# Performance work log

Hardware: AMD Instinct MI355X
Metric: run time of the kernel (lower is better)

The kernel has to match this reference:

```python
import jax, jax.numpy as jnp
import numpy as np

WIN = 12     # SAMv3 window_size
HEADS = 8    # num_heads

def _window(t, win=WIN):
    B, H, W, C = t.shape
    t = t.reshape(B, H // win, win, W // win, win, C).transpose(0, 1, 3, 2, 4, 5)
    return t.reshape(B, (H // win) * (W // win), win * win, C)

def _unwindow(t, H, W, win=WIN):
    B, nW, S, C = t.shape
    t = t.reshape(B, H // win, W // win, win, win, C).transpose(0, 1, 3, 2, 4, 5)
    return t.reshape(B, H, W, C)

def _sam(fq, fkv, bias, wq, wk, wv, wo, bo):
    # Windowed, masked cross-frame multi-head attention (SAMv3).
    # fq, fkv: (B, C, H, W); bias: (B, nW, 1, 1, S) additive mask bias.
    B, C, H, W = fq.shape
    hd = C // HEADS
    scale = hd ** -0.5
    q = _window(jnp.einsum('bchw,cd->bhwd', fq, wq))   # (B,nW,S,C)
    k = _window(jnp.einsum('bchw,cd->bhwd', fkv, wk))
    v = _window(jnp.einsum('bchw,cd->bhwd', fkv, wv))
    nW, S = q.shape[1], q.shape[2]
    q = q.reshape(B, nW, S, HEADS, hd)
    k = k.reshape(B, nW, S, HEADS, hd)
    v = v.reshape(B, nW, S, HEADS, hd)
    attn = jnp.einsum('bnqhd,bnkhd->bnhqk', q, k) * scale + bias
    attn = jax.nn.softmax(attn, axis=-1)
    out = jnp.einsum('bnhqk,bnkhd->bnqhd', attn, v).reshape(B, nW, S, C)
    out = out @ wo + bo
    return _unwindow(out, H, W).transpose(0, 3, 1, 2)  # (B, C, H, W)

def setup_inputs() -> dict:
    key = jax.random.key(0)
    B, C, T, H, W = 2, 384, 2, 192, 192
    ks = jax.random.split(key, 16)
    d = {}
    d['x'] = jax.random.normal(ks[0], (B, C, T, H, W), jnp.float32)
    d['mask'] = jax.random.randint(ks[1], (B, T, 1, H, W), 0, 2, jnp.int32)
    names = ['sam1_wq', 'sam1_wk', 'sam1_wv', 'sam1_wo',
             'sam2_wq', 'sam2_wk', 'sam2_wv', 'sam2_wo',
             'proj1_w', 'proj2_w']
    for i, n in enumerate(names):
        d[n] = jax.random.normal(ks[2 + i], (C, C), jnp.float32) * 0.02
    d['sam1_bo'] = jnp.zeros((C,), jnp.float32)
    d['sam2_bo'] = jnp.zeros((C,), jnp.float32)
    d['proj1_b'] = jnp.zeros((C,), jnp.float32)
    d['proj2_b'] = jnp.zeros((C,), jnp.float32)
    return d

def reference(x, mask, sam1_wq, sam1_wk, sam1_wv, sam1_wo, sam1_bo,
              sam2_wq, sam2_wk, sam2_wv, sam2_wo, sam2_bo,
              proj1_w, proj1_b, proj2_w, proj2_b):
    # x: (B, C, T=2, H, W); mask: (B, T, 1, H, W)
    f1 = x[:, :, 0]
    f2 = x[:, :, 1]
    m = mask[:, 1, 0][..., None]                      # (B, H, W, 1), frame-2 mask
    mw = _window(m)[..., 0]                           # (B, nW, S)
    bias = jnp.where(mw == 0, -1e9, 0.0).astype(x.dtype)[:, :, None, None, :]
    o1 = _sam(f1, f2, bias, sam1_wq, sam1_wk, sam1_wv, sam1_wo, sam1_bo)
    x1 = jnp.einsum('bchw,dc->bdhw', o1, proj1_w) + proj1_b[None, :, None, None]
    o2 = _sam(f2, f1, bias, sam2_wq, sam2_wk, sam2_wv, sam2_wo, sam2_bo)
    x2 = jnp.einsum('bchw,dc->bdhw', o2, proj2_w) + proj2_b[None, :, None, None]
    return jnp.concatenate([x1[:, :, None], x2[:, :, None]], axis=2)  # (B, C, 2, H, W)
```

## Files before the change

kernel.cpp:

```cpp
#include <hip/hip_runtime.h>
#include <stdint.h>

typedef __attribute__((ext_vector_type(8))) short bf16x8;
typedef __attribute__((ext_vector_type(4))) float f32x4;

#define HW    36864
#define CCH   384
#define NPIX  73728
#define W2    147456

__device__ __forceinline__ unsigned short f2bf(float f) {
  unsigned u = __builtin_bit_cast(unsigned, f);
  u += 0x7FFFu + ((u >> 16) & 1u);
  return (unsigned short)(u >> 16);
}

typedef const unsigned int __attribute__((address_space(1)))* gas1_t;
typedef unsigned int __attribute__((address_space(3)))* las3_t;
__device__ __forceinline__ void gload16(const void* g, void* l) {
  __builtin_amdgcn_global_load_lds((gas1_t)g, (las3_t)l, 16, 0, 0);
}


__global__ void k_wt(const float* __restrict__ w0, const float* __restrict__ w1,
                     const float* __restrict__ w2, const float* __restrict__ w3,
                     const float* __restrict__ w4, const float* __restrict__ w5,
                     unsigned short* __restrict__ wt) {
  int idx = blockIdx.x * 256 + threadIdx.x;
  int w = blockIdx.y;
  const float* W;
  switch (w) { case 0: W = w0; break; case 1: W = w1; break;
               case 2: W = w2; break; case 3: W = w3; break;
               case 4: W = w4; break; default: W = w5; break; }
  const int slotmap[6] = {0, 4, 5, 3, 1, 2};
  int slot = slotmap[w];
  int c = idx / 384, d = idx % 384;
  wt[(size_t)slot * W2 + (size_t)d * 384 + c] = f2bf(W[(size_t)c * 384 + d]);
}

__global__ void k_wf(const float* __restrict__ wo1, const float* __restrict__ pj1,
                     const float* __restrict__ wo2, const float* __restrict__ pj2,
                     unsigned short* __restrict__ wfT) {
  int idx = blockIdx.x * 256 + threadIdx.x;
  int s = blockIdx.y;
  const float* wo = s ? wo2 : wo1;
  const float* pj = s ? pj2 : pj1;
  int d = idx / 384, e = idx % 384;
  float acc = 0.f;
  for (int c = 0; c < 384; ++c) acc += pj[d * 384 + c] * wo[e * 384 + c];
  wfT[(size_t)s * W2 + (size_t)d * 384 + e] = f2bf(acc);
}

__global__ void k_bf(const float* __restrict__ bo1, const float* __restrict__ pj1,
                     const float* __restrict__ pb1, const float* __restrict__ bo2,
                     const float* __restrict__ pj2, const float* __restrict__ pb2,
                     float* __restrict__ bfused) {
  int t = threadIdx.x;
  int s = t / 384, d = t % 384;
  const float* bo = s ? bo2 : bo1;
  const float* pj = s ? pj2 : pj1;
  const float* pb = s ? pb2 : pb1;
  float acc = pb[d];
  for (int c = 0; c < 384; ++c) acc += pj[d * 384 + c] * bo[c];
  bfused[t] = acc;
}

__global__ __launch_bounds__(256) void k_tx(const float* __restrict__ x,
                                            unsigned short* __restrict__ xbf) {
  __shared__ float tile[64][65];
  int p0 = blockIdx.x * 64;
  int c0 = blockIdx.y * 64;
  int bt = blockIdx.z;
  int b = bt >> 1, t = bt & 1;
  int tid = threadIdx.x;
  int cl = tid >> 2;
  int pq = (tid & 3) * 4;
  const float* src = x + (((size_t)b * CCH + (c0 + cl)) * 2 + t) * HW + p0;
#pragma unroll
  for (int i = 0; i < 4; ++i) {
    int p_l = pq + i * 16;
    float4 v = *reinterpret_cast<const float4*>(src + p_l);
    tile[cl][p_l + 0] = v.x; tile[cl][p_l + 1] = v.y;
    tile[cl][p_l + 2] = v.z; tile[cl][p_l + 3] = v.w;
  }
  __syncthreads();
  int pl = tid >> 2;
  int cq = (tid & 3) * 16;
  unsigned short* dst = xbf + ((size_t)(t * 2 + b) * HW + p0 + pl) * CCH + c0 + cq;
  bf16x8 o0, o1;
#pragma unroll
  for (int j = 0; j < 8; ++j) o0[j] = (short)f2bf(tile[cq + j][pl]);
#pragma unroll
  for (int j = 0; j < 8; ++j) o1[j] = (short)f2bf(tile[cq + 8 + j][pl]);
  *reinterpret_cast<bf16x8*>(dst) = o0;
  *reinterpret_cast<bf16x8*>(dst + 8) = o1;
}

__global__ __launch_bounds__(512) void gemm_qkv(
    const unsigned short* __restrict__ xbf,
    const unsigned short* __restrict__ wt,
    unsigned short* __restrict__ qb0,
    unsigned short* __restrict__ qb1,
    unsigned short* __restrict__ kvb0,
    unsigned short* __restrict__ kvb1,
    float oscale) {
  __shared__ __align__(16) unsigned short Lsh[3][24576];
  const int tid = threadIdx.x;
  const int lane = tid & 63;
  const int wid = tid >> 6;
  const int wr = wid >> 1, wc = wid & 1;
  const int r15 = lane & 15, g = lane >> 4;

  const int gx = gridDim.x;
  const int nwg = gx * gridDim.y;
  const int bid = blockIdx.x + blockIdx.y * gx;
  const int chunk = nwg >> 3;
  const int l = (bid & 7) * chunk + (bid >> 3);
  const int bx = l % gx, by = l / gx;

  const int f = (by >= 288) ? 1 : 0;
  const int m0 = (by - f * 288) * 256;
  const int n0 = bx * 128;

  const unsigned short* A  = xbf + (size_t)f * NPIX * 384;
  const unsigned short* Bt = wt + (size_t)f * 3 * W2;
  unsigned short* Cq  = f ? qb1 : qb0;
  unsigned short* Ckv = f ? kvb0 : kvb1;

  const int gsl = (tid & 7) ^ ((tid >> 3) & 7);
  const unsigned short* srcA = A + (size_t)(m0 + (tid >> 3)) * 384 + gsl * 8;
  const unsigned short* srcB = Bt + (size_t)(n0 + (tid >> 3)) * 384 + gsl * 8;
  const int wu = tid & ~63;

  f32x4 acc[4][4];
  f32x4 zero4 = {0.f, 0.f, 0.f, 0.f};
#pragma unroll
  for (int a = 0; a < 4; ++a)
#pragma unroll
    for (int b = 0; b < 4; ++b) acc[a][b] = zero4;

#define STAGE_H0(buf, kt) do {                                         \
    size_t ko = (size_t)(kt) * 64;                                     \
    gload16(srcA + ko,            &Lsh[(buf)][(wu) * 8]);              \
    gload16(srcA + 64*384 + ko,   &Lsh[(buf)][(512 + wu) * 8]);        \
    gload16(srcB + ko,            &Lsh[(buf)][16384 + (wu) * 8]);      \
  } while (0)
#define STAGE_H1(buf, kt) do {                                         \
    size_t ko = (size_t)(kt) * 64;                                     \
    gload16(srcA + 128*384 + ko,  &Lsh[(buf)][(1024 + wu) * 8]);       \
    gload16(srcA + 192*384 + ko,  &Lsh[(buf)][(1536 + wu) * 8]);       \
    gload16(srcB + 64*384 + ko,   &Lsh[(buf)][16384 + (512 + wu) * 8]);\
  } while (0)

  const int rsw = r15 & 7;

#define PHASE(buf, ks, DO_STAGE, nbuf, kt2, END) do {                           \
    bf16x8 af[4], bfv[4];                                                       \
    _Pragma("unroll")                                                           \
    for (int a = 0; a < 4; ++a) {                                               \
      int row = wr * 64 + a * 16 + r15;                                         \
      af[a] = *(const bf16x8*)&Lsh[(buf)][row * 64 + (((ks)*4 + g) ^ rsw) * 8]; \
    }                                                                           \
    _Pragma("unroll")                                                           \
    for (int b = 0; b < 4; ++b) {                                               \
      int row = wc * 64 + b * 16 + r15;                                         \
      bfv[b] = *(const bf16x8*)&Lsh[(buf)][16384 + row * 64 + (((ks)*4 + g) ^ rsw) * 8];\
    }                                                                           \
    if (DO_STAGE == 1) STAGE_H0(nbuf, kt2);                                     \
    if (DO_STAGE == 2) STAGE_H1(nbuf, kt2);                                     \
    __builtin_amdgcn_s_barrier();                                               \
    asm volatile("s_waitcnt lgkmcnt(0)" ::: "memory");                          \
    __builtin_amdgcn_s_setprio(1);                                              \
    _Pragma("unroll")                                                           \
    for (int a = 0; a < 4; ++a)                                                 \
      _Pragma("unroll")                                                         \
      for (int b = 0; b < 4; ++b)                                               \
        acc[a][b] = __builtin_amdgcn_mfma_f32_16x16x32_bf16(af[a], bfv[b], acc[a][b], 0, 0, 0);\
    __builtin_amdgcn_s_setprio(0);                                              \
    if (END == 1) { asm volatile("s_waitcnt vmcnt(6)" ::: "memory"); }          \
    if (END != 2) { __builtin_amdgcn_s_barrier(); }                             \
  } while (0)

  STAGE_H0(0, 0); STAGE_H1(0, 0);
  STAGE_H0(1, 1); STAGE_H1(1, 1);
  asm volatile("s_waitcnt vmcnt(6)" ::: "memory");
  __builtin_amdgcn_s_barrier();

#pragma unroll
  for (int t = 0; t < 4; ++t) {
    const int buf = t % 3, nbuf = (t + 2) % 3;
    PHASE(buf, 0, 1, nbuf, t + 2, 0);
    PHASE(buf, 1, 2, nbuf, t + 2, 1);
  }
  PHASE(1, 0, 0, 0, 0, 0);
  PHASE(1, 1, 0, 0, 0, 2);
  __syncthreads();
  PHASE(2, 0, 0, 0, 0, 2);
  asm volatile("s_waitcnt lgkmcnt(0)" ::: "memory");
  PHASE(2, 1, 0, 0, 0, 2);
#undef STAGE_H0
#undef STAGE_H1
#undef PHASE

  unsigned short* Cp;
  int ldc2, ncol0;
  float sc;
  if (n0 < 384) { Cp = Cq;  ldc2 = 384; ncol0 = n0;       sc = oscale; }
  else          { Cp = Ckv; ldc2 = 768; ncol0 = n0 - 384; sc = 1.0f;   }
#pragma unroll
  for (int a = 0; a < 4; ++a) {
    size_t rbase = (size_t)(m0 + wr * 64 + a * 16 + g * 4) * ldc2;
#pragma unroll
    for (int b = 0; b < 4; ++b) {
      int n = ncol0 + wc * 64 + b * 16 + r15;
      unsigned short* cp = Cp + rbase + n;
#pragma unroll
      for (int r = 0; r < 4; ++r) cp[(size_t)r * ldc2] = f2bf(acc[a][b][r] * sc);
    }
  }
}

__global__ __launch_bounds__(256) void gemm_out(
    const unsigned short* __restrict__ wfT,
    const unsigned short* __restrict__ ob0,
    const unsigned short* __restrict__ ob1,
    float* __restrict__ Cf,
    const float* __restrict__ bfu) {
  __shared__ __align__(16) unsigned short Lsh[3][8192];
  const int tid = threadIdx.x;
  const int lane = tid & 63;
  const int wid = tid >> 6, wr = wid >> 1, wc = wid & 1;

  const int gx = gridDim.x, gy = gridDim.y;
  const int nwg = gx * gy * gridDim.z;
  const int bid = blockIdx.x + (blockIdx.y + blockIdx.z * gy) * gx;
  const int chunk = nwg >> 3;
  const int l = (bid & 7) * chunk + (bid >> 3);
  const int bx = l % gx;
  const int by = (l / gx) % gy;
  const int s  = l / (gx * gy);

  const unsigned short* A  = wfT + (size_t)s * W2;
  const unsigned short* Bt = s ? ob1 : ob0;
  const float* bias = bfu + s * 384;

  const int m0 = bx * 128;
  const int n0 = by * 128;
  const int r15 = lane & 15, g = lane >> 4;

  const int u1 = tid + 256;
  const unsigned short* srcA0 = A + (size_t)(m0 + (tid >> 2)) * 384 + (((tid & 3) ^ ((tid >> 3) & 3)) << 3);
  const unsigned short* srcA1 = A + (size_t)(m0 + (u1 >> 2)) * 384 + (((u1 & 3) ^ ((u1 >> 3) & 3)) << 3);
  const unsigned short* srcB0 = Bt + (size_t)(n0 + (tid >> 2)) * 384 + (((tid & 3) ^ ((tid >> 3) & 3)) << 3);
  const unsigned short* srcB1 = Bt + (size_t)(n0 + (u1 >> 2)) * 384 + (((u1 & 3) ^ ((u1 >> 3) & 3)) << 3);
  const int wbase = (tid & ~63) * 8;

  f32x4 acc[4][4];
  f32x4 zero4 = {0.f, 0.f, 0.f, 0.f};
#pragma unroll
  for (int a = 0; a < 4; ++a)
#pragma unroll
    for (int b = 0; b < 4; ++b) acc[a][b] = zero4;

  const int swzr = (g ^ ((r15 >> 1) & 3)) << 3;

#define STAGE(buf, kt) do {                                  \
    int ke = (kt) * 32;                                      \
    gload16(srcA0 + ke, &Lsh[(buf)][wbase]);                 \
    gload16(srcA1 + ke, &Lsh[(buf)][2048 + wbase]);          \
    gload16(srcB0 + ke, &Lsh[(buf)][4096 + wbase]);          \
    gload16(srcB1 + ke, &Lsh[(buf)][6144 + wbase]);          \
  } while (0)

#define COMPUTE(buf) do {                                                       \
    bf16x8 af[4], bfv[4];                                                       \
    _Pragma("unroll")                                                           \
    for (int a = 0; a < 4; ++a)                                                 \
      af[a] = *(const bf16x8*)&Lsh[(buf)][(wr * 64 + a * 16 + r15) * 32 + swzr];\
    _Pragma("unroll")                                                           \
    for (int b = 0; b < 4; ++b)                                                 \
      bfv[b] = *(const bf16x8*)&Lsh[(buf)][4096 + (wc * 64 + b * 16 + r15) * 32 + swzr];\
    _Pragma("unroll")                                                           \
    for (int a = 0; a < 4; ++a)                                                 \
      _Pragma("unroll")                                                         \
      for (int b = 0; b < 4; ++b)                                               \
        acc[a][b] = __builtin_amdgcn_mfma_f32_16x16x32_bf16(af[a], bfv[b], acc[a][b], 0, 0, 0);\
  } while (0)

  STAGE(0, 0);
  STAGE(1, 1);
#pragma unroll
  for (int kt = 0; kt < 11; ++kt) {
    asm volatile("s_waitcnt vmcnt(4)" ::: "memory");
    __builtin_amdgcn_s_barrier();
    asm volatile("" ::: "memory");
    if (kt < 10) STAGE((kt + 2) % 3, kt + 2);
    COMPUTE(kt % 3);
  }
  __syncthreads();
  COMPUTE(11 % 3);
#undef STAGE
#undef COMPUTE

  int bb = n0 / HW;
#pragma unroll
  for (int a = 0; a < 4; ++a) {
    int d = m0 + wr * 64 + a * 16 + g * 4;
#pragma unroll
    for (int b = 0; b < 4; ++b) {
      int n = n0 + wc * 64 + b * 16 + r15;
      int p = n - bb * HW;
#pragma unroll
      for (int r = 0; r < 4; ++r) {
        float v = acc[a][b][r] + bias[d + r];
        Cf[(((size_t)bb * CCH + (d + r)) * 2 + s) * HW + p] = v;
      }
    }
  }
}

__global__ __launch_bounds__(512, 2) void attn_kernel(
    const unsigned short* __restrict__ qb0,
    const unsigned short* __restrict__ qb1,
    const unsigned short* __restrict__ kvb0,
    const unsigned short* __restrict__ kvb1,
    const int* __restrict__ mask,
    unsigned short* __restrict__ ob0,
    unsigned short* __restrict__ ob1) {
  __shared__ __align__(16) unsigned short P[8][16][168];
  __shared__ int ptab[144];
  const int n = blockIdx.x, b = blockIdx.y, s = blockIdx.z;
  const unsigned short* q  = s ? qb1 : qb0;
  const unsigned short* kv = s ? kvb1 : kvb0;
  unsigned short* obuf = s ? ob1 : ob0;
  const int tid = threadIdx.x;
  const int h = tid >> 6, lane = tid & 63;
  const int c15 = lane & 15, g = lane >> 4;
  const int wy = n >> 4, wx = n & 15;
  const size_t rowbase = (size_t)b * HW;
  const int* mrow = mask + (size_t)(b * 2 + 1) * HW;

  if (tid < 144)
    ptab[tid] = (wy * 12 + tid / 12) * 192 + wx * 12 + tid % 12;

  for (int idx = lane; idx < 16 * 24; idx += 64)
    P[h][idx / 24][144 + (idx % 24)] = 0;
  __syncthreads();

  float biasv[9];
#pragma unroll
  for (int nt = 0; nt < 9; ++nt)
    biasv[nt] = (mrow[ptab[nt * 16 + c15]] == 0) ? -1e9f : 0.0f;

  bf16x8 zfrag = {0, 0, 0, 0, 0, 0, 0, 0};
  f32x4 zero4 = {0.f, 0.f, 0.f, 0.f};

  bf16x8 kf0[9], kf1[9];
#pragma unroll
  for (int nt = 0; nt < 9; ++nt) {
    const unsigned short* kp = kv + (rowbase + ptab[nt * 16 + c15]) * 768 + h * 48;
    kf0[nt] = *(const bf16x8*)(kp + g * 8);
    kf1[nt] = zfrag;
    if (g < 2) kf1[nt] = *(const bf16x8*)(kp + 32 + g * 8);
  }

  const unsigned short* vb = kv + rowbase * 768 + 384 + h * 48;
  bf16x8 vf[5][3];
#pragma unroll
  for (int ks = 0; ks < 5; ++ks) {
#pragma unroll
    for (int dt = 0; dt < 3; ++dt) {
      bf16x8 v = {0, 0, 0, 0, 0, 0, 0, 0};
#pragma unroll
      for (int j = 0; j < 8; ++j) {
        int sk = ks * 32 + g * 8 + j;
        if (sk < 144)
          v[j] = (short)vb[(size_t)ptab[sk] * 768 + dt * 16 + c15];
      }
      vf[ks][dt] = v;
    }
  }

  bf16x8 qf0, qf1;
  {
    const unsigned short* qp = q + (rowbase + ptab[c15]) * 384 + h * 48;
    qf0 = *(const bf16x8*)(qp + g * 8);
    qf1 = zfrag;
    if (g < 2) qf1 = *(const bf16x8*)(qp + 32 + g * 8);
  }

  for (int mt = 0; mt < 9; ++mt) {
    bf16x8 qn0 = zfrag, qn1 = zfrag;
    if (mt < 8) {
      const unsigned short* qp = q + (rowbase + ptab[(mt + 1) * 16 + c15]) * 384 + h * 48;
      qn0 = *(const bf16x8*)(qp + g * 8);
      if (g < 2) qn1 = *(const bf16x8*)(qp + 32 + g * 8);
    }

    float l4[4] = {0.f, 0.f, 0.f, 0.f};
    f32x4 oacc[3];
#pragma unroll
    for (int dt = 0; dt < 3; ++dt) oacc[dt] = zero4;

#pragma unroll
    for (int nt = 0; nt < 9; ++nt) {
      f32x4 sv = __builtin_amdgcn_mfma_f32_16x16x32_bf16(qf1, kf1[nt], zero4, 0, 0, 0);
      sv = __builtin_amdgcn_mfma_f32_16x16x32_bf16(qf0, kf0[nt], sv, 0, 0, 0);
#pragma unroll
      for (int r = 0; r < 4; ++r) {
        float pv = __expf(sv[r] + biasv[nt]);
        l4[r] += pv;
        P[h][g * 4 + r][nt * 16 + c15] = f2bf(pv);
      }
      if (nt & 1) {
        int ks = nt >> 1;
        bf16x8 pf = *(const bf16x8*)&P[h][c15][ks * 32 + g * 8];
#pragma unroll
        for (int dt = 0; dt < 3; ++dt)
          oacc[dt] = __builtin_amdgcn_mfma_f32_16x16x32_bf16(pf, vf[ks][dt], oacc[dt], 0, 0, 0);
      }
    }
    {
      bf16x8 pf = *(const bf16x8*)&P[h][c15][4 * 32 + g * 8];
#pragma unroll
      for (int dt = 0; dt < 3; ++dt)
        oacc[dt] = __builtin_amdgcn_mfma_f32_16x16x32_bf16(pf, vf[4][dt], oacc[dt], 0, 0, 0);
    }

#pragma unroll
    for (int st = 1; st < 16; st <<= 1)
#pragma unroll
      for (int r = 0; r < 4; ++r) l4[r] += __shfl_xor(l4[r], st, 64);

    float inv[4];
#pragma unroll
    for (int r = 0; r < 4; ++r) inv[r] = 1.0f / l4[r];
#pragma unroll
    for (int dt = 0; dt < 3; ++dt) {
#pragma unroll
      for (int r = 0; r < 4; ++r) {
        int so = mt * 16 + g * 4 + r;
        obuf[(rowbase + ptab[so]) * 384 + h * 48 + dt * 16 + c15] =
            f2bf(oacc[dt][r] * inv[r]);
      }
    }

    qf0 = qn0; qf1 = qn1;
  }
}

extern "C" void kernel_launch(void* const* d_in, const int* in_sizes, int n_in,
                              void* d_out, int out_size, void* d_ws, size_t ws_size,
                              hipStream_t stream) {
  const float* x    = (const float*)d_in[0];
  const int*   mask = (const int*)d_in[1];
  const float* wq1 = (const float*)d_in[2];
  const float* wk1 = (const float*)d_in[3];
  const float* wv1 = (const float*)d_in[4];
  const float* wo1 = (const float*)d_in[5];
  const float* wq2 = (const float*)d_in[6];
  const float* wk2 = (const float*)d_in[7];
  const float* wv2 = (const float*)d_in[8];
  const float* wo2 = (const float*)d_in[9];
  const float* pj1 = (const float*)d_in[10];
  const float* pj2 = (const float*)d_in[11];
  const float* bo1 = (const float*)d_in[12];
  const float* bo2 = (const float*)d_in[13];
  const float* pb1 = (const float*)d_in[14];
  const float* pb2 = (const float*)d_in[15];
  float* out = (float*)d_out;

  const float SCALE = 0.14433756729740643f;

  char* ws = (char*)d_ws;
  size_t off = 0;
  unsigned short* wt   = (unsigned short*)(ws + off); off += (size_t)6 * W2 * 2;
  unsigned short* wfT  = (unsigned short*)(ws + off); off += (size_t)2 * W2 * 2;
  float*          bfu  = (float*)(ws + off);          off += (size_t)2 * 384 * 4;
  unsigned short* xbf  = (unsigned short*)(ws + off); off += (size_t)4 * HW * CCH * 2;
  size_t qsz = (size_t)NPIX * 384 * 2, kvsz = (size_t)NPIX * 768 * 2;
  unsigned short* qb0  = (unsigned short*)(ws + off); off += qsz;
  unsigned short* qb1  = (unsigned short*)(ws + off); off += qsz;
  unsigned short* kvb0 = (unsigned short*)(ws + off); off += kvsz;
  unsigned short* kvb1 = (unsigned short*)(ws + off); off += kvsz;
  unsigned short* ob0  = (unsigned short*)(ws + off); off += qsz;
  unsigned short* ob1  = (unsigned short*)(ws + off); off += qsz;
  if (ws_size < off) return;

  k_wt<<<dim3(576, 6), 256, 0, stream>>>(wq1, wk1, wv1, wq2, wk2, wv2, wt);
  k_wf<<<dim3(576, 2), 256, 0, stream>>>(wo1, pj1, wo2, pj2, wfT);
  k_bf<<<1, 768, 0, stream>>>(bo1, pj1, pb1, bo2, pj2, pb2, bfu);
  k_tx<<<dim3(576, 6, 4), 256, 0, stream>>>(x, xbf);

  gemm_qkv<<<dim3(9, 576), 512, 0, stream>>>(xbf, wt, qb0, qb1, kvb0, kvb1, SCALE);
  attn_kernel<<<dim3(256, 2, 2), 512, 0, stream>>>(qb0, qb1, kvb0, kvb1, mask, ob0, ob1);
  gemm_out<<<dim3(3, 576, 2), 256, 0, stream>>>(wfT, ob0, ob1, out, bfu);
}
```

Baseline: 682.2 us.

## Enlarge QKV GEMM tile to 256x256 with padded weights and double buffering

Reshapes the QKV projection GEMM to use 256x256 output tiles, with 8 waves in a 2x4 arrangement, instead of 256x128. The weight matrix is laid out per frame as a contiguous 1152-row block, zero-padded to 1280 rows by a new padding kernel. The LDS pipeline changes from triple buffering to double buffering, with finer interleaving of loads and MFMA quarters. The aim is fewer reloads of the activation matrix across column blocks, at the cost of padded wasted MFMA work, higher register pressure and more barriers.

```diff
diff --git a/kernel.cpp b/kernel.cpp
--- a/kernel.cpp
+++ b/kernel.cpp
@@ -8,6 +8,8 @@
 #define CCH   384
 #define NPIX  73728
 #define W2    147456
+#define NPAD  1280
+#define WTF   491520
 
 __device__ __forceinline__ unsigned short f2bf(float f) {
   unsigned u = __builtin_bit_cast(unsigned, f);
@@ -32,10 +34,17 @@
   switch (w) { case 0: W = w0; break; case 1: W = w1; break;
                case 2: W = w2; break; case 3: W = w3; break;
                case 4: W = w4; break; default: W = w5; break; }
-  const int slotmap[6] = {0, 4, 5, 3, 1, 2};
-  int slot = slotmap[w];
+  const int fmap[6]    = {0, 1, 1, 1, 0, 0};
+  const int basemap[6] = {0, 384, 768, 0, 384, 768};
   int c = idx / 384, d = idx % 384;
-  wt[(size_t)slot * W2 + (size_t)d * 384 + c] = f2bf(W[(size_t)c * 384 + d]);
+  wt[(size_t)fmap[w] * WTF + (size_t)(basemap[w] + d) * 384 + c] =
+      f2bf(W[(size_t)c * 384 + d]);
+}
+
+__global__ void k_pad(unsigned short* __restrict__ wt) {
+  int idx = blockIdx.x * 256 + threadIdx.x;
+  int f = idx / 49152, rem = idx % 49152;
+  wt[(size_t)f * WTF + 1152 * 384 + rem] = 0;
 }
 
 __global__ void k_wf(const float* __restrict__ wo1, const float* __restrict__ pj1,
@@ -104,12 +113,13 @@
     unsigned short* __restrict__ kvb0,
     unsigned short* __restrict__ kvb1,
     float oscale) {
-  __shared__ __align__(16) unsigned short Lsh[3][24576];
+  __shared__ __align__(16) unsigned short Lsh[2][32768];
   const int tid = threadIdx.x;
   const int lane = tid & 63;
   const int wid = tid >> 6;
-  const int wr = wid >> 1, wc = wid & 1;
+  const int wr = wid >> 2, wc = wid & 3;
   const int r15 = lane & 15, g = lane >> 4;
+  const int rsw = r15 & 7;
 
   const int gx = gridDim.x;
   const int nwg = gx * gridDim.y;
@@ -120,102 +130,117 @@
 
   const int f = (by >= 288) ? 1 : 0;
   const int m0 = (by - f * 288) * 256;
-  const int n0 = bx * 128;
+  const int n0 = bx * 256;
 
   const unsigned short* A  = xbf + (size_t)f * NPIX * 384;
-  const unsigned short* Bt = wt + (size_t)f * 3 * W2;
+  const unsigned short* Bt = wt + (size_t)f * WTF;
   unsigned short* Cq  = f ? qb1 : qb0;
   unsigned short* Ckv = f ? kvb0 : kvb1;
 
   const int gsl = (tid & 7) ^ ((tid >> 3) & 7);
   const unsigned short* srcA = A + (size_t)(m0 + (tid >> 3)) * 384 + gsl * 8;
   const unsigned short* srcB = Bt + (size_t)(n0 + (tid >> 3)) * 384 + gsl * 8;
-  const int wu = tid & ~63;
-
-  f32x4 acc[4][4];
+
+  f32x4 acc[8][4];
   f32x4 zero4 = {0.f, 0.f, 0.f, 0.f};
 #pragma unroll
-  for (int a = 0; a < 4; ++a)
+  for (int a = 0; a < 8; ++a)
 #pragma unroll
     for (int b = 0; b < 4; ++b) acc[a][b] = zero4;
 
-#define STAGE_H0(buf, kt) do {                                         \
-    size_t ko = (size_t)(kt) * 64;                                     \
-    gload16(srcA + ko,            &Lsh[(buf)][(wu) * 8]);              \
-    gload16(srcA + 64*384 + ko,   &Lsh[(buf)][(512 + wu) * 8]);        \
-    gload16(srcB + ko,            &Lsh[(buf)][16384 + (wu) * 8]);      \
+#define SA(buf, kt, q) gload16(srcA + (size_t)(q) * 64 * 384 + (kt) * 64, \
+                               &Lsh[(buf)][tid * 8 + (q) * 4096])
+#define SB(buf, kt, q) gload16(srcB + (size_t)(q) * 64 * 384 + (kt) * 64, \
+                               &Lsh[(buf)][16384 + tid * 8 + (q) * 4096])
+
+  bf16x8 af[4][2], bf[2][2];
+#define LDA(buf, mh) do {                                                        \
+    _Pragma("unroll")                                                            \
+    for (int a = 0; a < 4; ++a) {                                                \
+      int row = wr * 128 + (mh) * 64 + a * 16 + r15;                             \
+      af[a][0] = *(const bf16x8*)&Lsh[(buf)][row * 64 + ((0 + g) ^ rsw) * 8];    \
+      af[a][1] = *(const bf16x8*)&Lsh[(buf)][row * 64 + ((4 + g) ^ rsw) * 8];    \
+    } } while (0)
+#define LDB(buf, nh) do {                                                        \
+    _Pragma("unroll")                                                            \
+    for (int b = 0; b < 2; ++b) {                                                \
+      int row = wc * 64 + (nh) * 32 + b * 16 + r15;                              \
+      bf[b][0] = *(const bf16x8*)&Lsh[(buf)][16384 + row * 64 + ((0 + g) ^ rsw) * 8];\
+      bf[b][1] = *(const bf16x8*)&Lsh[(buf)][16384 + row * 64 + ((4 + g) ^ rsw) * 8];\
+    } } while (0)
+#define MM(mh, nh) do {                                                          \
+    __builtin_amdgcn_s_setprio(1);                                               \
+    _Pragma("unroll")                                                            \
+    for (int a = 0; a < 4; ++a)                                                  \
+      _Pragma("unroll")                                                          \
+      for (int b = 0; b < 2; ++b) {                                              \
+        acc[(mh)*4+a][(nh)*2+b] = __builtin_amdgcn_mfma_f32_16x16x32_bf16(       \
+            af[a][0], bf[b][0], acc[(mh)*4+a][(nh)*2+b], 0, 0, 0);               \
+        acc[(mh)*4+a][(nh)*2+b] = __builtin_amdgcn_mfma_f32_16x16x32_bf16(       \
+            af[a][1], bf[b][1], acc[(mh)*4+a][(nh)*2+b], 0, 0, 0);               \
+      }                                                                          \
+    __builtin_amdgcn_s_setprio(0);                                               \
   } while (0)
-#define STAGE_H1(buf, kt) do {                                         \
-    size_t ko = (size_t)(kt) * 64;                                     \
-    gload16(srcA + 128*384 + ko,  &Lsh[(buf)][(1024 + wu) * 8]);       \
-    gload16(srcA + 192*384 + ko,  &Lsh[(buf)][(1536 + wu) * 8]);       \
-    gload16(srcB + 64*384 + ko,   &Lsh[(buf)][16384 + (512 + wu) * 8]);\
+
+#define BAR() __builtin_amdgcn_s_barrier()
+#define LGKM0() asm volatile("s_waitcnt lgkmcnt(0)" ::: "memory")
+
+  SB(0, 0, 0); SB(0, 0, 1); SB(0, 0, 2); SB(0, 0, 3);
+  SA(0, 0, 0); SA(0, 0, 2);
+  SA(0, 0, 1); SA(0, 0, 3);
+  asm volatile("s_waitcnt vmcnt(2)" ::: "memory");
+  BAR();
+
+#define TILE(kt, STG, W1STR, W3)                                              \
+  do {                                                                        \
+    const int c_ = (kt) & 1, s_ = c_ ^ 1;                                     \
+    LDA(c_, 0); LDB(c_, 0);                                                   \
+    if (STG) { SB(s_, (kt) + 1, 0); SB(s_, (kt) + 1, 1); }                    \
+    BAR(); LGKM0(); MM(0, 0); BAR();                                          \
+    LDB(c_, 1);                                                               \
+    if (STG) { SB(s_, (kt) + 1, 2); SB(s_, (kt) + 1, 3); }                    \
+    BAR(); LGKM0(); MM(0, 1);                                                 \
+    asm volatile("s_waitcnt " W1STR ::: "memory");                            \
+    BAR();                                                                    \
+    LDA(c_, 1);                                                               \
+    if (STG) { SA(s_, (kt) + 1, 0); SA(s_, (kt) + 1, 2); }                    \
+    BAR(); LGKM0(); MM(1, 1); BAR();                                          \
+    LDB(c_, 0);                                                               \
+    if (STG) { SA(s_, (kt) + 1, 1); SA(s_, (kt) + 1, 3); }                    \
+    BAR(); LGKM0(); MM(1, 0);                                                 \
+    if (W3) { asm volatile("s_waitcnt vmcnt(2)" ::: "memory"); BAR(); }       \
   } while (0)
 
-  const int rsw = r15 & 7;
-
-#define PHASE(buf, ks, DO_STAGE, nbuf, kt2, END) do {                           \
-    bf16x8 af[4], bfv[4];                                                       \
-    _Pragma("unroll")                                                           \
-    for (int a = 0; a < 4; ++a) {                                               \
-      int row = wr * 64 + a * 16 + r15;                                         \
-      af[a] = *(const bf16x8*)&Lsh[(buf)][row * 64 + (((ks)*4 + g) ^ rsw) * 8]; \
-    }                                                                           \
-    _Pragma("unroll")                                                           \
-    for (int b = 0; b < 4; ++b) {                                               \
-      int row = wc * 64 + b * 16 + r15;                                         \
-      bfv[b] = *(const bf16x8*)&Lsh[(buf)][16384 + row * 64 + (((ks)*4 + g) ^ rsw) * 8];\
-    }                                                                           \
-    if (DO_STAGE == 1) STAGE_H0(nbuf, kt2);                                     \
-    if (DO_STAGE == 2) STAGE_H1(nbuf, kt2);                                     \
-    __builtin_amdgcn_s_barrier();                                               \
-    asm volatile("s_waitcnt lgkmcnt(0)" ::: "memory");                          \
-    __builtin_amdgcn_s_setprio(1);                                              \
-    _Pragma("unroll")                                                           \
-    for (int a = 0; a < 4; ++a)                                                 \
-      _Pragma("unroll")                                                         \
-      for (int b = 0; b < 4; ++b)                                               \
-        acc[a][b] = __builtin_amdgcn_mfma_f32_16x16x32_bf16(af[a], bfv[b], acc[a][b], 0, 0, 0);\
-    __builtin_amdgcn_s_setprio(0);                                              \
-    if (END == 1) { asm volatile("s_waitcnt vmcnt(6)" ::: "memory"); }          \
-    if (END != 2) { __builtin_amdgcn_s_barrier(); }                             \
-  } while (0)
-
-  STAGE_H0(0, 0); STAGE_H1(0, 0);
-  STAGE_H0(1, 1); STAGE_H1(1, 1);
-  asm volatile("s_waitcnt vmcnt(6)" ::: "memory");
-  __builtin_amdgcn_s_barrier();
-
-#pragma unroll
-  for (int t = 0; t < 4; ++t) {
-    const int buf = t % 3, nbuf = (t + 2) % 3;
-    PHASE(buf, 0, 1, nbuf, t + 2, 0);
-    PHASE(buf, 1, 2, nbuf, t + 2, 1);
-  }
-  PHASE(1, 0, 0, 0, 0, 0);
-  PHASE(1, 1, 0, 0, 0, 2);
-  __syncthreads();
-  PHASE(2, 0, 0, 0, 0, 2);
-  asm volatile("s_waitcnt lgkmcnt(0)" ::: "memory");
-  PHASE(2, 1, 0, 0, 0, 2);
-#undef STAGE_H0
-#undef STAGE_H1
-#undef PHASE
-
-  unsigned short* Cp;
-  int ldc2, ncol0;
-  float sc;
-  if (n0 < 384) { Cp = Cq;  ldc2 = 384; ncol0 = n0;       sc = oscale; }
-  else          { Cp = Ckv; ldc2 = 768; ncol0 = n0 - 384; sc = 1.0f;   }
-#pragma unroll
-  for (int a = 0; a < 4; ++a) {
-    size_t rbase = (size_t)(m0 + wr * 64 + a * 16 + g * 4) * ldc2;
+  TILE(0, 1, "vmcnt(4)", 1);
+  TILE(1, 1, "vmcnt(4)", 1);
+  TILE(2, 1, "vmcnt(4)", 1);
+  TILE(3, 1, "vmcnt(4)", 1);
+  TILE(4, 1, "vmcnt(4)", 1);
+  TILE(5, 0, "vmcnt(0)", 0);
+#undef TILE
+#undef SA
+#undef SB
+#undef LDA
+#undef LDB
+#undef MM
+#undef BAR
+#undef LGKM0
+
+#pragma unroll
+  for (int a = 0; a < 8; ++a) {
+    int m = m0 + wr * 128 + a * 16 + g * 4;
 #pragma unroll
     for (int b = 0; b < 4; ++b) {
-      int n = ncol0 + wc * 64 + b * 16 + r15;
-      unsigned short* cp = Cp + rbase + n;
-#pragma unroll
-      for (int r = 0; r < 4; ++r) cp[(size_t)r * ldc2] = f2bf(acc[a][b][r] * sc);
+      int nbase = n0 + wc * 64 + b * 16;
+      if (nbase < 384) {
+        unsigned short* cp = Cq + (size_t)m * 384 + nbase + r15;
+#pragma unroll
+        for (int r = 0; r < 4; ++r) cp[(size_t)r * 384] = f2bf(acc[a][b][r] * oscale);
+      } else if (nbase < 1152) {
+        unsigned short* cp = Ckv + (size_t)m * 768 + (nbase - 384) + r15;
+#pragma unroll
+        for (int r = 0; r < 4; ++r) cp[(size_t)r * 768] = f2bf(acc[a][b][r]);
+      }
     }
   }
 }
@@ -474,7 +499,7 @@
 
   char* ws = (char*)d_ws;
   size_t off = 0;
-  unsigned short* wt   = (unsigned short*)(ws + off); off += (size_t)6 * W2 * 2;
+  unsigned short* wt   = (unsigned short*)(ws + off); off += (size_t)2 * WTF * 2;
   unsigned short* wfT  = (unsigned short*)(ws + off); off += (size_t)2 * W2 * 2;
   float*          bfu  = (float*)(ws + off);          off += (size_t)2 * 384 * 4;
   unsigned short* xbf  = (unsigned short*)(ws + off); off += (size_t)4 * HW * CCH * 2;
@@ -488,11 +513,12 @@
   if (ws_size < off) return;
 
   k_wt<<<dim3(576, 6), 256, 0, stream>>>(wq1, wk1, wv1, wq2, wk2, wv2, wt);
+  k_pad<<<384, 256, 0, stream>>>(wt);
   k_wf<<<dim3(576, 2), 256, 0, stream>>>(wo1, pj1, wo2, pj2, wfT);
   k_bf<<<1, 768, 0, stream>>>(bo1, pj1, pb1, bo2, pj2, pb2, bfu);
   k_tx<<<dim3(576, 6, 4), 256, 0, stream>>>(x, xbf);
 
-  gemm_qkv<<<dim3(9, 576), 512, 0, stream>>>(xbf, wt, qb0, qb1, kvb0, kvb1, SCALE);
+  gemm_qkv<<<dim3(5, 576), 512, 0, stream>>>(xbf, wt, qb0, qb1, kvb0, kvb1, SCALE);
   attn_kernel<<<dim3(256, 2, 2), 512, 0, stream>>>(qb0, qb1, kvb0, kvb1, mask, ob0, ob1);
   gemm_out<<<dim3(3, 576, 2), 256, 0, stream>>>(wfT, ob0, ob1, out, bfu);
 }
```

Result: faster. 661.5 us (-3.0%).
